# Kernel tuning notes

Hardware: AMD Instinct MI355X
Metric: run time of the kernel (lower is better)

## Reference

```python
import jax, jax.numpy as jnp
import numpy as np

VOCAB, EMB, B, L, H, OUT = 100000, 300, 2048, 200, 128, 20

def setup_inputs() -> dict:
    key = jax.random.key(0)
    ks = jax.random.split(key, 7)
    x = jax.random.randint(ks[0], (B, L), 0, VOCAB, dtype=jnp.int64 if jax.config.read('jax_enable_x64') else jnp.int32)
    lengths = jax.random.randint(ks[1], (B,), 1, L + 1, dtype=x.dtype)  # avoid zero length
    emb_table = jax.random.normal(ks[2], (VOCAB, EMB), dtype=jnp.float32)
    W1 = jax.random.normal(ks[3], (EMB, H), dtype=jnp.float32) * (1.0 / np.sqrt(EMB))
    b1 = jax.random.normal(ks[4], (H,), dtype=jnp.float32) * 0.01
    W2 = jax.random.normal(ks[5], (H, OUT), dtype=jnp.float32) * (1.0 / np.sqrt(H))
    b2 = jax.random.normal(ks[6], (OUT,), dtype=jnp.float32) * 0.01
    return {"x": x, "lengths": lengths, "emb_table": emb_table,
            "W1": W1, "b1": b1, "W2": W2, "b2": b2}

def reference(x, lengths, emb_table, W1, b1, W2, b2):
    # embedding lookup: [B, L, EMB]
    emb = emb_table[x]
    # faithful to original: sum over FULL sequence, divide by per-sample length
    rep = emb.sum(axis=1) / lengths.astype(emb.dtype)[:, None]  # [B, EMB]
    h = jax.nn.relu(rep @ W1 + b1)                              # [B, H]
    logits = h @ W2 + b2                                        # [B, OUT]
    return logits
```

## Files before the change

kernel.cpp:

```cpp
#include <hip/hip_runtime.h>

typedef _Float16 f16;
typedef _Float16 f16x8 __attribute__((ext_vector_type(8)));
typedef float    f32x4 __attribute__((ext_vector_type(4)));

#define VOCAB 100000
#define BB   2048
#define LL   200
#define EMB  300
#define HH   128
#define OUTD 20
#define RPW  50
#define KPAD 320

#define FGI(hl, nt, ks, l, j) (((((hl) * 8 + (nt)) * 10 + (ks)) * 64 + (l)) * 8 + (j))
#define W1F_ELEMS (2 * 8 * 10 * 64 * 8)

__global__ void w1f_prep(const float* __restrict__ W1,
                         f16* __restrict__ w1f)
{
    const int n = blockIdx.x;
    const int k = threadIdx.x;
    const float v = (k < EMB) ? W1[(size_t)k * HH + n] : 0.f;
    const f16 hi = (f16)v;
    const f16 lo = (f16)(v - (float)hi);
    const int nt = n >> 4;
    const int ks = k >> 5;
    const int kk = k & 31;
    const int lane = ((kk >> 3) << 4) | (n & 15);
    const int j = kk & 7;
    w1f[FGI(0, nt, ks, lane, j)] = hi;
    w1f[FGI(1, nt, ks, lane, j)] = lo;
}

#define BMv8 64
#define NBLK ((VOCAB + BMv8 - 1) / BMv8)

#define AFI(mt, ks, l) ((((mt) * 10 + (ks)) * 64 + (l)) * 8)
#define PSW 136

__global__ __launch_bounds__(256, 4) void proj_mfma(
    const float* __restrict__ table,
    const f16*   __restrict__ w1f,
    f16*         __restrict__ P)
{
    alignas(16) __shared__ f16 Af[4 * 10 * 64 * 8];

    const int t    = threadIdx.x;
    const int w    = t >> 6;
    const int lane = t & 63;
    const int row0 = blockIdx.x * BMv8;

    const int kg   = lane >> 4;
    const int arow = row0 + w * 16 + (lane & 15);
    const bool aok = (arow < VOCAB);
    const float* ap = table + (size_t)arow * EMB + kg * 8;

    float4 sa[10][2];
    #pragma unroll
    for (int i = 0; i < 10; ++i) {
        const int k = 32 * i + 8 * kg;
        const float4 z = make_float4(0.f, 0.f, 0.f, 0.f);
        sa[i][0] = (aok && k + 4 <= EMB) ? *(const float4*)(ap + 32 * i)     : z;
        sa[i][1] = (aok && k + 8 <= EMB) ? *(const float4*)(ap + 32 * i + 4) : z;
    }
    #pragma unroll
    for (int i = 0; i < 10; ++i) {
        const float v[8] = {sa[i][0].x, sa[i][0].y, sa[i][0].z, sa[i][0].w,
                            sa[i][1].x, sa[i][1].y, sa[i][1].z, sa[i][1].w};
        f16x8 h;
        #pragma unroll
        for (int j = 0; j < 8; ++j) h[j] = (f16)v[j];
        *(f16x8*)&Af[AFI(w, i, lane)] = h;
    }
    __syncthreads();

    f32x4 acc[4][2];
    #pragma unroll
    for (int i = 0; i < 4; ++i)
        #pragma unroll
        for (int j = 0; j < 2; ++j) acc[i][j] = (f32x4)0.f;

    const int ntb = 2 * w;

    const f16* bh0p = w1f + FGI(0, ntb,     0, lane, 0);
    const f16* bh1p = w1f + FGI(0, ntb + 1, 0, lane, 0);
    const f16* bl0p = w1f + FGI(1, ntb,     0, lane, 0);
    const f16* bl1p = w1f + FGI(1, ntb + 1, 0, lane, 0);
    const int KSTRIDE = 64 * 8;

    f16x8 cb0 = *(const f16x8*)(bh0p);
    f16x8 cb1 = *(const f16x8*)(bh1p);
    f16x8 cb2 = *(const f16x8*)(bl0p);
    f16x8 cb3 = *(const f16x8*)(bl1p);

    for (int ks = 0; ks < 10; ++ks) {
        f16x8 nb0, nb1, nb2, nb3;
        if (ks + 1 < 10) {
            const int o = (ks + 1) * KSTRIDE;
            nb0 = *(const f16x8*)(bh0p + o);
            nb1 = *(const f16x8*)(bh1p + o);
            nb2 = *(const f16x8*)(bl0p + o);
            nb3 = *(const f16x8*)(bl1p + o);
        }

        f16x8 a[4];
        #pragma unroll
        for (int m4 = 0; m4 < 4; ++m4)
            a[m4] = *(const f16x8*)&Af[AFI(m4, ks, lane)];

        #pragma unroll
        for (int m4 = 0; m4 < 4; ++m4) {
            acc[m4][0] = __builtin_amdgcn_mfma_f32_16x16x32_f16(a[m4], cb0, acc[m4][0], 0, 0, 0);
            acc[m4][0] = __builtin_amdgcn_mfma_f32_16x16x32_f16(a[m4], cb2, acc[m4][0], 0, 0, 0);
            acc[m4][1] = __builtin_amdgcn_mfma_f32_16x16x32_f16(a[m4], cb1, acc[m4][1], 0, 0, 0);
            acc[m4][1] = __builtin_amdgcn_mfma_f32_16x16x32_f16(a[m4], cb3, acc[m4][1], 0, 0, 0);
        }
        cb0 = nb0; cb1 = nb1; cb2 = nb2; cb3 = nb3;
    }

    __syncthreads();
    f16* Ps = Af;
    #pragma unroll
    for (int m4 = 0; m4 < 4; ++m4) {
        const int rb = m4 * 16 + 4 * (lane >> 4);
        #pragma unroll
        for (int n2 = 0; n2 < 2; ++n2) {
            const int col = (ntb + n2) * 16 + (lane & 15);
            const f32x4 v = acc[m4][n2];
            #pragma unroll
            for (int j = 0; j < 4; ++j)
                Ps[(rb + j) * PSW + col] = (f16)v[j];
        }
    }
    __syncthreads();

    {
        const int srow = t >> 2;
        const int sc   = (t & 3) * 32;
        const int grow = row0 + srow;
        if (grow < VOCAB) {
            f16* dst = P + (size_t)grow * HH + sc;
            const f16* src = Ps + srow * PSW + sc;
            #pragma unroll
            for (int m = 0; m < 4; ++m)
                *(f16x8*)(dst + 8 * m) = *(const f16x8*)(src + 8 * m);
        }
    }
}

__global__ __launch_bounds__(256) void gather_mlp(
    const int*   __restrict__ x,
    const int*   __restrict__ lengths,
    const f16*   __restrict__ P,
    const float* __restrict__ b1,
    const float* __restrict__ W2,
    const float* __restrict__ b2,
    float*       __restrict__ out)
{
    __shared__ float part_s[16][HH];
    __shared__ float h_s[HH];

    const int b    = blockIdx.x;
    const int t    = threadIdx.x;
    const int lane = t & 63;
    const int w    = t >> 6;

    const int myidx = (lane < RPW) ? x[b * LL + RPW * w + lane] : 0;

    const int c = lane & 15;
    const size_t coff = (size_t)c * 8;

    int rid[13];
    #pragma unroll
    for (int i = 0; i < 12; ++i) {
        const int r0 = __builtin_amdgcn_readlane(myidx, 4 * i + 0);
        const int r1 = __builtin_amdgcn_readlane(myidx, 4 * i + 1);
        const int r2 = __builtin_amdgcn_readlane(myidx, 4 * i + 2);
        const int r3 = __builtin_amdgcn_readlane(myidx, 4 * i + 3);
        const int rlo = (lane & 16) ? r1 : r0;
        const int rhi = (lane & 16) ? r3 : r2;
        rid[i] = (lane & 32) ? rhi : rlo;
    }
    {
        const int r0 = __builtin_amdgcn_readlane(myidx, 48);
        const int r1 = __builtin_amdgcn_readlane(myidx, 49);
        rid[12] = (lane & 16) ? r1 : r0;
    }

    f16x8 vb[13];
    #pragma unroll
    for (int i = 0; i < 13; ++i)
        vb[i] = *(const f16x8*)(P + (size_t)rid[i] * HH + coff);

    float acc[8];
    #pragma unroll
    for (int j = 0; j < 8; ++j) acc[j] = 0.f;
    #pragma unroll
    for (int i = 0; i < 12; ++i)
        #pragma unroll
        for (int j = 0; j < 8; ++j) acc[j] += (float)vb[i][j];
    if (lane < 32) {
        #pragma unroll
        for (int j = 0; j < 8; ++j) acc[j] += (float)vb[12][j];
    }

    *(float4*)&part_s[t >> 4][c * 8]     = make_float4(acc[0], acc[1], acc[2], acc[3]);
    *(float4*)&part_s[t >> 4][c * 8 + 4] = make_float4(acc[4], acc[5], acc[6], acc[7]);
    __syncthreads();

    const float inv_len = 1.0f / (float)lengths[b];
    if (t < HH) {
        float s = 0.f;
        #pragma unroll
        for (int p = 0; p < 16; ++p) s += part_s[p][t];
        h_s[t] = fmaxf(fmaf(s, inv_len, b1[t]), 0.f);
    }
    __syncthreads();

    if (t < OUTD) {
        float o = b2[t];
        #pragma unroll
        for (int k = 0; k < HH; ++k)
            o = fmaf(h_s[k], W2[k * OUTD + t], o);
        out[b * OUTD + t] = o;
    }
}

#define NSRT 256
__global__ __launch_bounds__(256) void fused_dnn(
    const int*   __restrict__ x,
    const int*   __restrict__ lengths,
    const float* __restrict__ table,
    const float* __restrict__ W1,
    const float* __restrict__ b1,
    const float* __restrict__ W2,
    const float* __restrict__ b2,
    float*       __restrict__ out)
{
    __shared__ int    idx_s[NSRT];
    __shared__ float4 part_s[4][76];
    __shared__ float  rep_s[EMB];
    __shared__ float  h_part[2][HH];
    __shared__ float  h_s[HH];

    const int b    = blockIdx.x;
    const int t    = threadIdx.x;
    const int w    = t >> 6;
    const int lane = t & 63;

    idx_s[t] = (t < LL) ? x[b * LL + t] : 0x7FFFFFFF;
    __syncthreads();

    #pragma unroll
    for (int k = 2; k <= NSRT; k <<= 1) {
        #pragma unroll
        for (int j = k >> 1; j > 0; j >>= 1) {
            const int ixj = t ^ j;
            if (ixj > t) {
                const int a0 = idx_s[t];
                const int a1 = idx_s[ixj];
                const bool up = ((t & k) == 0);
                if ((a0 > a1) == up) { idx_s[t] = a1; idx_s[ixj] = a0; }
            }
            __syncthreads();
        }
    }

    const int myidx = (lane < RPW) ? idx_s[w + 4 * lane] : 0;

    float4 acc_a = make_float4(0.f, 0.f, 0.f, 0.f);
    float4 acc_b = make_float4(0.f, 0.f, 0.f, 0.f);
    const bool hasb = (lane < (EMB / 4 - 64));

    #pragma unroll 5
    for (int i = 0; i < RPW; ++i) {
        const int ridx = __builtin_amdgcn_readlane(myidx, i);
        const float4* row = (const float4*)(table + (size_t)ridx * EMB);
        float4 va = row[lane];
        acc_a.x += va.x; acc_a.y += va.y; acc_a.z += va.z; acc_a.w += va.w;
        if (hasb) {
            float4 vb = row[64 + lane];
            acc_b.x += vb.x; acc_b.y += vb.y; acc_b.z += vb.z; acc_b.w += vb.w;
        }
    }

    part_s[w][lane] = acc_a;
    if (hasb) part_s[w][64 + lane] = acc_b;
    __syncthreads();

    const float inv_len = 1.0f / (float)lengths[b];
    const float* ps = (const float*)part_s;
    {
        float s = ps[t] + ps[304 + t] + ps[608 + t] + ps[912 + t];
        rep_s[t] = s * inv_len;
    }
    if (t < (EMB - 256)) {
        int c = 256 + t;
        float s = ps[c] + ps[304 + c] + ps[608 + c] + ps[912 + c];
        rep_s[c] = s * inv_len;
    }
    __syncthreads();

    {
        const int half = t >> 7;
        const int col  = t & 127;
        float hacc = (half == 0) ? b1[col] : 0.0f;
        const int k0 = half * (EMB / 2);
        #pragma unroll 5
        for (int k = k0; k < k0 + EMB / 2; ++k)
            hacc = fmaf(rep_s[k], W1[k * HH + col], hacc);
        h_part[half][col] = hacc;
    }
    __syncthreads();
    if (t < HH)
        h_s[t] = fmaxf(h_part[0][t] + h_part[1][t], 0.0f);
    __syncthreads();

    if (t < OUTD) {
        float oacc = b2[t];
        #pragma unroll
        for (int k = 0; k < HH; ++k)
            oacc = fmaf(h_s[k], W2[k * OUTD + t], oacc);
        out[b * OUTD + t] = oacc;
    }
}

extern "C" void kernel_launch(void* const* d_in, const int* in_sizes, int n_in,
                              void* d_out, int out_size, void* d_ws, size_t ws_size,
                              hipStream_t stream) {
    const int*   x       = (const int*)  d_in[0];
    const int*   lengths = (const int*)  d_in[1];
    const float* table   = (const float*)d_in[2];
    const float* W1      = (const float*)d_in[3];
    const float* b1      = (const float*)d_in[4];
    const float* W2      = (const float*)d_in[5];
    const float* b2      = (const float*)d_in[6];
    float*       out     = (float*)d_out;

    const size_t PELEMS = (size_t)VOCAB * HH;
    const size_t NEED   = (PELEMS + W1F_ELEMS) * sizeof(f16);

    if (d_ws != nullptr && ws_size >= NEED) {
        f16* P   = (f16*)d_ws;
        f16* w1f = P + PELEMS;
        w1f_prep<<<HH, KPAD, 0, stream>>>(W1, w1f);
        proj_mfma<<<NBLK, 256, 0, stream>>>(table, w1f, P);
        gather_mlp<<<BB, 256, 0, stream>>>(x, lengths, P, b1, W2, b2, out);
    } else {
        fused_dnn<<<BB, 256, 0, stream>>>(x, lengths, table, W1, b1, W2, b2, out);
    }
}
```

Measured before the change: 234.0 us.

## Make projection kernel persistent with double-buffered table panel prefetch

The projection kernel now launches a fixed grid of 512 blocks that loop over 64-row table panels. Each block prefetches the next panel's fp32 rows into registers while it runs MFMAs on the current panel, then converts and writes them into a second LDS buffer. This is meant to hide global load latency behind compute in a kernel bound by streaming the table. In exchange, LDS use doubles, the launch bound drops to 2 blocks per CU, and the 80 floats of prefetch registers per thread may limit occupancy.

```diff
diff --git a/kernel.cpp b/kernel.cpp
--- a/kernel.cpp
+++ b/kernel.cpp
@@ -34,118 +34,128 @@
 }
 
 #define BMv8 64
-#define NBLK ((VOCAB + BMv8 - 1) / BMv8)
+#define NPANELS ((VOCAB + BMv8 - 1) / BMv8)
+#define GRIDP 512
 
 #define AFI(mt, ks, l) ((((mt) * 10 + (ks)) * 64 + (l)) * 8)
 #define PSW 136
 
-__global__ __launch_bounds__(256, 4) void proj_mfma(
+__global__ __launch_bounds__(256, 2) void proj_mfma(
     const float* __restrict__ table,
     const f16*   __restrict__ w1f,
     f16*         __restrict__ P)
 {
-    alignas(16) __shared__ f16 Af[4 * 10 * 64 * 8];
+    alignas(16) __shared__ f16 Af[2][4 * 10 * 64 * 8];
 
     const int t    = threadIdx.x;
     const int w    = t >> 6;
     const int lane = t & 63;
-    const int row0 = blockIdx.x * BMv8;
-
     const int kg   = lane >> 4;
-    const int arow = row0 + w * 16 + (lane & 15);
-    const bool aok = (arow < VOCAB);
-    const float* ap = table + (size_t)arow * EMB + kg * 8;
-
-    float4 sa[10][2];
-    #pragma unroll
-    for (int i = 0; i < 10; ++i) {
-        const int k = 32 * i + 8 * kg;
-        const float4 z = make_float4(0.f, 0.f, 0.f, 0.f);
-        sa[i][0] = (aok && k + 4 <= EMB) ? *(const float4*)(ap + 32 * i)     : z;
-        sa[i][1] = (aok && k + 8 <= EMB) ? *(const float4*)(ap + 32 * i + 4) : z;
-    }
-    #pragma unroll
-    for (int i = 0; i < 10; ++i) {
-        const float v[8] = {sa[i][0].x, sa[i][0].y, sa[i][0].z, sa[i][0].w,
-                            sa[i][1].x, sa[i][1].y, sa[i][1].z, sa[i][1].w};
-        f16x8 h;
-        #pragma unroll
-        for (int j = 0; j < 8; ++j) h[j] = (f16)v[j];
-        *(f16x8*)&Af[AFI(w, i, lane)] = h;
-    }
-    __syncthreads();
-
-    f32x4 acc[4][2];
-    #pragma unroll
-    for (int i = 0; i < 4; ++i)
-        #pragma unroll
-        for (int j = 0; j < 2; ++j) acc[i][j] = (f32x4)0.f;
+    const int rsub = w * 16 + (lane & 15);
 
     const int ntb = 2 * w;
-
     const f16* bh0p = w1f + FGI(0, ntb,     0, lane, 0);
     const f16* bh1p = w1f + FGI(0, ntb + 1, 0, lane, 0);
     const f16* bl0p = w1f + FGI(1, ntb,     0, lane, 0);
     const f16* bl1p = w1f + FGI(1, ntb + 1, 0, lane, 0);
     const int KSTRIDE = 64 * 8;
 
-    f16x8 cb0 = *(const f16x8*)(bh0p);
-    f16x8 cb1 = *(const f16x8*)(bh1p);
-    f16x8 cb2 = *(const f16x8*)(bl0p);
-    f16x8 cb3 = *(const f16x8*)(bl1p);
-
-    for (int ks = 0; ks < 10; ++ks) {
-        f16x8 nb0, nb1, nb2, nb3;
-        if (ks + 1 < 10) {
-            const int o = (ks + 1) * KSTRIDE;
-            nb0 = *(const f16x8*)(bh0p + o);
-            nb1 = *(const f16x8*)(bh1p + o);
-            nb2 = *(const f16x8*)(bl0p + o);
-            nb3 = *(const f16x8*)(bl1p + o);
-        }
-
-        f16x8 a[4];
-        #pragma unroll
-        for (int m4 = 0; m4 < 4; ++m4)
-            a[m4] = *(const f16x8*)&Af[AFI(m4, ks, lane)];
-
-        #pragma unroll
-        for (int m4 = 0; m4 < 4; ++m4) {
-            acc[m4][0] = __builtin_amdgcn_mfma_f32_16x16x32_f16(a[m4], cb0, acc[m4][0], 0, 0, 0);
-            acc[m4][0] = __builtin_amdgcn_mfma_f32_16x16x32_f16(a[m4], cb2, acc[m4][0], 0, 0, 0);
-            acc[m4][1] = __builtin_amdgcn_mfma_f32_16x16x32_f16(a[m4], cb1, acc[m4][1], 0, 0, 0);
-            acc[m4][1] = __builtin_amdgcn_mfma_f32_16x16x32_f16(a[m4], cb3, acc[m4][1], 0, 0, 0);
-        }
-        cb0 = nb0; cb1 = nb1; cb2 = nb2; cb3 = nb3;
-    }
-
-    __syncthreads();
-    f16* Ps = Af;
-    #pragma unroll
-    for (int m4 = 0; m4 < 4; ++m4) {
-        const int rb = m4 * 16 + 4 * (lane >> 4);
-        #pragma unroll
-        for (int n2 = 0; n2 < 2; ++n2) {
-            const int col = (ntb + n2) * 16 + (lane & 15);
-            const f32x4 v = acc[m4][n2];
-            #pragma unroll
-            for (int j = 0; j < 4; ++j)
-                Ps[(rb + j) * PSW + col] = (f16)v[j];
-        }
-    }
-    __syncthreads();
-
-    {
-        const int srow = t >> 2;
-        const int sc   = (t & 3) * 32;
-        const int grow = row0 + srow;
-        if (grow < VOCAB) {
-            f16* dst = P + (size_t)grow * HH + sc;
-            const f16* src = Ps + srow * PSW + sc;
-            #pragma unroll
-            for (int m = 0; m < 4; ++m)
-                *(f16x8*)(dst + 8 * m) = *(const f16x8*)(src + 8 * m);
-        }
+    float4 sa[10][2];
+
+    auto LOADA = [&](int panel) {
+        const int arow = panel * BMv8 + rsub;
+        const bool aok = (arow < VOCAB);
+        const float* ap = table + (size_t)arow * EMB + kg * 8;
+        #pragma unroll
+        for (int i = 0; i < 10; ++i) {
+            const int k = 32 * i + 8 * kg;
+            const float4 z = make_float4(0.f, 0.f, 0.f, 0.f);
+            sa[i][0] = (aok && k + 4 <= EMB) ? *(const float4*)(ap + 32 * i)     : z;
+            sa[i][1] = (aok && k + 8 <= EMB) ? *(const float4*)(ap + 32 * i + 4) : z;
+        }
+    };
+    auto CVTWRITE = [&](int buf) {
+        #pragma unroll
+        for (int i = 0; i < 10; ++i) {
+            const float v[8] = {sa[i][0].x, sa[i][0].y, sa[i][0].z, sa[i][0].w,
+                                sa[i][1].x, sa[i][1].y, sa[i][1].z, sa[i][1].w};
+            f16x8 h;
+            #pragma unroll
+            for (int j = 0; j < 8; ++j) h[j] = (f16)v[j];
+            *(f16x8*)&Af[buf][AFI(w, i, lane)] = h;
+        }
+    };
+
+    int p = blockIdx.x;
+    LOADA(p);
+    CVTWRITE(0);
+    __syncthreads();
+    int cur = 0;
+
+    while (p < NPANELS) {
+        const int pn = p + GRIDP;
+        const bool hasnext = (pn < NPANELS);
+        if (hasnext) LOADA(pn);
+
+        f32x4 acc[4][2];
+        #pragma unroll
+        for (int i = 0; i < 4; ++i)
+            #pragma unroll
+            for (int j = 0; j < 2; ++j) acc[i][j] = (f32x4)0.f;
+
+        #pragma unroll
+        for (int ks = 0; ks < 10; ++ks) {
+            const int o = ks * KSTRIDE;
+            const f16x8 cb0 = *(const f16x8*)(bh0p + o);
+            const f16x8 cb1 = *(const f16x8*)(bh1p + o);
+            const f16x8 cb2 = *(const f16x8*)(bl0p + o);
+            const f16x8 cb3 = *(const f16x8*)(bl1p + o);
+            f16x8 a[4];
+            #pragma unroll
+            for (int m4 = 0; m4 < 4; ++m4)
+                a[m4] = *(const f16x8*)&Af[cur][AFI(m4, ks, lane)];
+            #pragma unroll
+            for (int m4 = 0; m4 < 4; ++m4) {
+                acc[m4][0] = __builtin_amdgcn_mfma_f32_16x16x32_f16(a[m4], cb0, acc[m4][0], 0, 0, 0);
+                acc[m4][0] = __builtin_amdgcn_mfma_f32_16x16x32_f16(a[m4], cb2, acc[m4][0], 0, 0, 0);
+                acc[m4][1] = __builtin_amdgcn_mfma_f32_16x16x32_f16(a[m4], cb1, acc[m4][1], 0, 0, 0);
+                acc[m4][1] = __builtin_amdgcn_mfma_f32_16x16x32_f16(a[m4], cb3, acc[m4][1], 0, 0, 0);
+            }
+        }
+        __syncthreads();
+
+        {
+            f16* Ps = &Af[cur][0];
+            #pragma unroll
+            for (int m4 = 0; m4 < 4; ++m4) {
+                const int rb = m4 * 16 + 4 * (lane >> 4);
+                #pragma unroll
+                for (int n2 = 0; n2 < 2; ++n2) {
+                    const int col = (ntb + n2) * 16 + (lane & 15);
+                    const f32x4 v = acc[m4][n2];
+                    #pragma unroll
+                    for (int j = 0; j < 4; ++j)
+                        Ps[(rb + j) * PSW + col] = (f16)v[j];
+                }
+            }
+        }
+        if (hasnext) CVTWRITE(cur ^ 1);
+        __syncthreads();
+
+        {
+            const int srow = t >> 2;
+            const int sc   = (t & 3) * 32;
+            const int grow = p * BMv8 + srow;
+            if (grow < VOCAB) {
+                f16* dst = P + (size_t)grow * HH + sc;
+                const f16* src = &Af[cur][0] + srow * PSW + sc;
+                #pragma unroll
+                for (int m = 0; m < 4; ++m)
+                    *(f16x8*)(dst + 8 * m) = *(const f16x8*)(src + 8 * m);
+            }
+        }
+        p = pn;
+        cur ^= 1;
     }
 }
 
@@ -345,7 +355,7 @@
         f16* P   = (f16*)d_ws;
         f16* w1f = P + PELEMS;
         w1f_prep<<<HH, KPAD, 0, stream>>>(W1, w1f);
-        proj_mfma<<<NBLK, 256, 0, stream>>>(table, w1f, P);
+        proj_mfma<<<GRIDP, 256, 0, stream>>>(table, w1f, P);
         gather_mlp<<<BB, 256, 0, stream>>>(x, lengths, P, b1, W2, b2, out);
     } else {
         fused_dnn<<<BB, 256, 0, stream>>>(x, lengths, table, W1, b1, W2, b2, out);
```

After: 292.6 us. 25.1% more time.
